# Optimization experiments

Measured on AMD Instinct MI355X. Metric: run time of the kernel, lower is better.

## Reference

```python
import jax, jax.numpy as jnp
import numpy as np
import math

B, S, D_MODEL = 2, 2048, 1024
H = 16
DK = D_MODEL // H          # 64, down-proj per-stream dim
NOPE, ROPE = 128, 64
D_HEAD = NOPE + ROPE       # 192 = d_latent // H
D_LATENT = H * D_HEAD      # 3072
ROT_DIM = 2 * ((ROPE // 2) // 2)  # rotary dim actually rotated = qk_rope_dim//2 = 32
EPS = 1e-6


def _rmsnorm(x, w):
    out = x * jax.lax.rsqrt(jnp.mean(x * x, axis=-1, keepdims=True) + EPS)
    return out * w


def _apply_rope(x):
    # x: [b, h, s, d]; rotate first ROT_DIM channels, interleaved pairing
    s = x.shape[-2]
    inv_freq = 1.0 / (10000.0 ** (jnp.arange(0, ROT_DIM, 2, dtype=jnp.float32) / ROT_DIM))
    freqs = jnp.arange(s, dtype=jnp.float32)[:, None] * inv_freq[None, :]  # [s, ROT_DIM//2]
    freqs = jnp.repeat(freqs, 2, axis=-1)  # [s, ROT_DIM], (f0,f0,f1,f1,...)
    cos, sin = jnp.cos(freqs), jnp.sin(freqs)
    xl, xr = x[..., :ROT_DIM], x[..., ROT_DIM:]
    x1, x2 = xl[..., 0::2], xl[..., 1::2]
    rot = jnp.stack([-x2, x1], axis=-1).reshape(xl.shape)
    xl = xl * cos + rot * sin
    return jnp.concatenate([xl, xr], axis=-1)


def setup_inputs() -> dict:
    key = jax.random.key(0)
    ks = jax.random.split(key, 5)
    sc = 0.02
    x = jax.random.normal(ks[0], (B, S, D_MODEL), jnp.float32)
    mask = jnp.broadcast_to(jnp.tril(jnp.ones((S, S), jnp.int32)), (B, S, S))
    w_down = jax.random.normal(ks[1], (D_MODEL, 3 * DK), jnp.float32) * sc
    rms_w = jnp.ones((3 * DK,), jnp.float32)
    w_up = jax.random.normal(ks[2], (3 * DK, 3 * D_LATENT), jnp.float32) * sc
    w_o = jax.random.normal(ks[3], (D_LATENT, D_MODEL), jnp.float32) * sc
    return {"x": x, "mask": mask, "w_down": w_down, "rms_w": rms_w, "w_up": w_up, "w_o": w_o}


def reference(x, mask, w_down, rms_w, w_up, w_o):
    h = x @ w_down                        # [b, s, 3*dk]
    h = _rmsnorm(h, rms_w)
    qkv = h @ w_up                        # [b, s, 3*d_latent]
    q, k, v = jnp.split(qkv, 3, axis=-1)  # each [b, s, d_latent]

    def to_heads(t):
        # einops '(d h)': d outer, h inner
        return t.reshape(B, S, D_HEAD, H).transpose(0, 3, 1, 2)  # [b, h, s, d]

    q, k, v = to_heads(q), to_heads(k), to_heads(v)
    q_nope, q_rope = q[..., :NOPE], q[..., NOPE:]
    k_nope, k_rope = k[..., :NOPE], k[..., NOPE:]
    q_rope = _apply_rope(q_rope)
    k_rope = _apply_rope(k_rope)

    scores = (jnp.einsum('bhid,bhjd->bhij', q_nope, k_nope)
              + jnp.einsum('bhid,bhjd->bhij', q_rope, k_rope))
    scores = scores / math.sqrt(NOPE + ROPE)
    scores = jnp.where(mask[:, None] == 0, -1e9, scores)
    attn = jax.nn.softmax(scores, axis=-1)

    out = jnp.einsum('bhij,bhjd->bhid', attn, v)        # [b, h, s, d]
    out = out.transpose(0, 2, 1, 3).reshape(B, S, D_LATENT)  # 'b h s d -> b s (h d)'
    return out @ w_o
```

## Files before the change

kernel.cpp:

```cpp
#include <hip/hip_runtime.h>
#include <stdint.h>
#include <stddef.h>


typedef __bf16 bf16x8 __attribute__((ext_vector_type(8)));
typedef float  f32x4  __attribute__((ext_vector_type(4)));

#define MFMA16x16(a,b,c) __builtin_amdgcn_mfma_f32_16x16x32_bf16((a),(b),(c),0,0,0)

__device__ __forceinline__ uint16_t f2bf(float f){
  union { float f; uint32_t u; } v; v.f = f;
  uint32_t u = v.u + 0x7fffu + ((v.u >> 16) & 1u);
  return (uint16_t)(u >> 16);
}
__device__ __forceinline__ bf16x8 load_frag(const uint16_t* p){
  uint4 u = *reinterpret_cast<const uint4*>(p);
  return __builtin_bit_cast(bf16x8, u);
}
__device__ __forceinline__ f32x4 fzero(){
  f32x4 z = {0.f, 0.f, 0.f, 0.f};
  return z;
}
__device__ __forceinline__ uint32_t pack2(float a, float b){
  return (uint32_t)f2bf(a) | ((uint32_t)f2bf(b) << 16);
}
__device__ __forceinline__ void gl2lds16(const uint16_t* g, uint16_t* l){
  __builtin_amdgcn_global_load_lds(
      (const __attribute__((address_space(1))) uint32_t*)g,
      (__attribute__((address_space(3))) uint32_t*)l,
      16, 0, 0);
}

__global__ __launch_bounds__(256) void k_transpose_cvt(const float* __restrict__ in,
                                                       uint16_t* __restrict__ out,
                                                       int R, int C){
  __shared__ float t[32][33];
  const int tc = blockIdx.x * 32;
  const int tr = blockIdx.y * 32;
  const int j = threadIdx.x & 31, i0 = threadIdx.x >> 5;
  for(int ii = 0; ii < 4; ++ii){
    int r = i0 + ii * 8;
    t[r][j] = in[(size_t)(tr + r) * C + tc + j];
  }
  __syncthreads();
  for(int ii = 0; ii < 4; ++ii){
    int c = i0 + ii * 8;
    out[(size_t)(tc + c) * R + tr + j] = f2bf(t[j][c]);
  }
}

__global__ __launch_bounds__(256) void k_down_mfma(const float* __restrict__ x,
                                                   const uint16_t* __restrict__ wdt,
                                                   const float* __restrict__ rms_w,
                                                   uint16_t* __restrict__ h_out){
  __shared__ __align__(16) uint16_t as[32 * 64];
  __shared__ float hsq[32];
  const int tid  = threadIdx.x;
  const int wave = tid >> 6, lane = tid & 63;
  const int ml = lane & 15, qd = lane >> 4;
  const int m0 = blockIdx.x * 32;
  const int n0w = wave * 48;
  if(tid < 32) hsq[tid] = 0.f;

  f32x4 acc[2][3];
#pragma unroll
  for(int mt = 0; mt < 2; ++mt)
#pragma unroll
    for(int nt = 0; nt < 3; ++nt) acc[mt][nt] = fzero();

  const int srow = tid >> 3, sc = tid & 7;
  for(int kt = 0; kt < 16; ++kt){
    const float* src = x + (size_t)(m0 + srow) * 1024 + kt * 64 + sc * 8;
    float4 a = *reinterpret_cast<const float4*>(src);
    float4 b = *reinterpret_cast<const float4*>(src + 4);
    uint4 pk;
    pk.x = pack2(a.x, a.y); pk.y = pack2(a.z, a.w);
    pk.z = pack2(b.x, b.y); pk.w = pack2(b.z, b.w);
    __syncthreads();
    *reinterpret_cast<uint4*>(as + srow * 64 + ((sc ^ (srow & 7)) * 8)) = pk;
    __syncthreads();
#pragma unroll
    for(int kk = 0; kk < 2; ++kk){
      bf16x8 af[2];
#pragma unroll
      for(int mt = 0; mt < 2; ++mt){
        int row = mt * 16 + ml;
        af[mt] = load_frag(as + row * 64 + (((kk * 4 + qd) ^ (row & 7)) * 8));
      }
#pragma unroll
      for(int nt = 0; nt < 3; ++nt){
        bf16x8 bfr = load_frag(wdt + (size_t)(n0w + nt * 16 + ml) * 1024 + kt * 64 + kk * 32 + qd * 8);
#pragma unroll
        for(int mt = 0; mt < 2; ++mt)
          acc[mt][nt] = MFMA16x16(af[mt], bfr, acc[mt][nt]);
      }
    }
  }
  __syncthreads();
#pragma unroll
  for(int mt = 0; mt < 2; ++mt)
#pragma unroll
    for(int r = 0; r < 4; ++r){
      float s = acc[mt][0][r]*acc[mt][0][r] + acc[mt][1][r]*acc[mt][1][r] + acc[mt][2][r]*acc[mt][2][r];
#pragma unroll
      for(int off = 1; off < 16; off <<= 1) s += __shfl_xor(s, off);
      if(ml == 0) atomicAdd(&hsq[mt * 16 + qd * 4 + r], s);
    }
  __syncthreads();
  float rw[3];
#pragma unroll
  for(int nt = 0; nt < 3; ++nt) rw[nt] = rms_w[n0w + nt * 16 + ml];
#pragma unroll
  for(int mt = 0; mt < 2; ++mt)
#pragma unroll
    for(int r = 0; r < 4; ++r){
      int row = mt * 16 + qd * 4 + r;
      float scl = rsqrtf(hsq[row] * (1.0f / 192.0f) + 1e-6f);
#pragma unroll
      for(int nt = 0; nt < 3; ++nt)
        h_out[(size_t)(m0 + row) * 192 + n0w + nt * 16 + ml] = f2bf(acc[mt][nt][r] * scl * rw[nt]);
    }
}

__global__ __launch_bounds__(256) void k_gemm_up(const uint16_t* __restrict__ hmat,
                                                 const uint16_t* __restrict__ wt,
                                                 uint16_t* __restrict__ q_t,
                                                 uint16_t* __restrict__ k_t,
                                                 uint16_t* __restrict__ v_t){
  __shared__ __align__(16) uint16_t rp[16 * 129 * 8];
  const int wave = threadIdx.x >> 6, lane = threadIdx.x & 63;
  const int ml = lane & 15, qd = lane >> 4;
  const int m0 = blockIdx.y * 32;
  const int bx = blockIdx.x;
  const int which = bx / 6;
  const int d0b = (bx % 6) * 32;
  const int n0w = bx * 512 + wave * 128;
  const int d0w = d0b + wave * 8;

  bf16x8 af[2][6];
#pragma unroll
  for(int mt = 0; mt < 2; ++mt)
#pragma unroll
    for(int kk = 0; kk < 6; ++kk)
      af[mt][kk] = load_frag(hmat + (size_t)(m0 + mt * 16 + ml) * 192 + kk * 32 + qd * 8);

  f32x4 acc[8][2];
#pragma unroll
  for(int nt = 0; nt < 8; ++nt){ acc[nt][0] = fzero(); acc[nt][1] = fzero(); }
#pragma unroll
  for(int nt = 0; nt < 8; ++nt){
#pragma unroll
    for(int kk = 0; kk < 6; ++kk){
      bf16x8 b = load_frag(wt + (size_t)(n0w + nt * 16 + ml) * 192 + kk * 32 + qd * 8);
      acc[nt][0] = MFMA16x16(af[0][kk], b, acc[nt][0]);
      acc[nt][1] = MFMA16x16(af[1][kk], b, acc[nt][1]);
    }
  }

  const int b   = m0 >> 11;
  const int s0  = m0 & 2047;
  const int kt2 = s0 >> 6;
  const int row0 = s0 & 63;
  uint4* rp4 = (uint4*)rp;

  if(which < 2){
    const float qs = which ? 1.0f : 0.07216878364870322f;
    const bool rope = (d0w >= 128) && (d0w < 160);
#pragma unroll
    for(int mt = 0; mt < 2; ++mt)
#pragma unroll
      for(int r = 0; r < 4; ++r){
        int t = mt * 16 + qd * 4 + r;
        int s = s0 + t;
        float v[8];
#pragma unroll
        for(int nt = 0; nt < 8; ++nt) v[nt] = acc[nt][mt][r] * qs;
        if(rope){
#pragma unroll
          for(int pi = 0; pi < 4; ++pi){
            int fi = (d0w + 2 * pi - 128) >> 1;
            float invf = __expf(-(float)fi * 0.5756462732485114f);
            float sn, cs;
            sincosf((float)s * invf, &sn, &cs);
            float e = v[2 * pi], o = v[2 * pi + 1];
            v[2 * pi]     = e * cs - o * sn;
            v[2 * pi + 1] = o * cs + e * sn;
          }
        }
        uint4 pk;
        pk.x = pack2(v[0], v[1]); pk.y = pack2(v[2], v[3]);
        pk.z = pack2(v[4], v[5]); pk.w = pack2(v[6], v[7]);
        rp4[ml * 129 + t * 4 + (wave ^ (t & 3))] = pk;
      }
  } else {
#pragma unroll
    for(int nt = 0; nt < 8; ++nt){
      int dl = wave * 8 + nt;
#pragma unroll
      for(int mt = 0; mt < 2; ++mt){
        int jc = mt * 2 + (qd >> 1);
        int slot = ml * 129 + dl * 4 + (jc ^ (dl & 3));
        uint2 pk;
        pk.x = pack2(acc[nt][mt][0], acc[nt][mt][1]);
        pk.y = pack2(acc[nt][mt][2], acc[nt][mt][3]);
        *(reinterpret_cast<uint2*>(rp + slot * 8) + (qd & 1)) = pk;
      }
    }
  }
  __syncthreads();

  if(which < 2){
    uint16_t* dst = which ? k_t : q_t;
    const int cb = d0b >> 3;
#pragma unroll
    for(int it = 0; it < 8; ++it){
      int h = wave * 4 + (it & 3), rhalf = it >> 2;
      int tloc = rhalf * 16 + (lane >> 2), p = lane & 3;
      int row = row0 + tloc;
      uint4 val = rp4[h * 129 + tloc * 4 + p];
      size_t off = ((size_t)(b * 16 + h) * 32 + kt2) * 12288
                 + (size_t)row * 192 + ((cb ^ (tloc & 4)) + p) * 8;
      *reinterpret_cast<uint4*>(dst + off) = val;
    }
  } else {
    const int cs0 = row0 >> 3;
#pragma unroll
    for(int it = 0; it < 8; ++it){
      int h = wave * 4 + (it & 3), dhalf = it >> 2;
      int dl = dhalf * 16 + (lane >> 2), p = lane & 3;
      uint4 val = rp4[h * 129 + dl * 4 + p];
      size_t off = ((size_t)(b * 16 + h) * 32 + kt2) * 12288
                 + (size_t)(d0b + dl) * 64 + ((cs0 ^ (dl & 4)) + p) * 8;
      *reinterpret_cast<uint4*>(v_t + off) = val;
    }
  }
}

__global__ __launch_bounds__(256, 3) void k_attn(const uint16_t* __restrict__ q_t,
                                                 const uint16_t* __restrict__ k_t,
                                                 const uint16_t* __restrict__ v_t,
                                                 uint16_t* __restrict__ attn_out){
  __shared__ __align__(16) uint16_t ks[64 * 192];
  __shared__ __align__(16) uint16_t vs[208 * 64];
  const int tid  = threadIdx.x;
  const int wave = tid >> 6;
  const int lane = tid & 63;
  const int ml   = lane & 15;
  const int qd   = lane >> 4;
  const int L    = blockIdx.x;
  const int idx  = L >> 3;
  const int qt   = 31 - (idx & 31);
  const int bh   = (L & 7) + ((idx >> 5) << 3);

  {
    uint32_t* vw = (uint32_t*)vs;
    vw[6144 + tid] = 0x3F803F80u;
    vw[6400 + tid] = 0x3F803F80u;
  }

  {
    const uint16_t* qtile = q_t + ((size_t)bh * 32 + qt) * (64 * 192);
#pragma unroll
    for(int it = 0; it < 6; ++it){
      int seg = it * 4 + wave;
      gl2lds16(qtile + seg * 512 + lane * 8, ks + seg * 512);
    }
  }
  __syncthreads();
  bf16x8 qf[6];
  {
    int row = wave * 16 + ml;
#pragma unroll
    for(int kk = 0; kk < 6; ++kk)
      qf[kk] = load_frag(ks + row * 192 + (((kk * 4 + qd) ^ (row & 7)) * 8));
  }

  f32x4 o[13];
#pragma unroll
  for(int i = 0; i < 13; ++i) o[i] = fzero();

  for(int kt = 0; kt <= qt; ++kt){
    __syncthreads();
    const uint16_t* ktile = k_t + ((size_t)bh * 32 + kt) * (64 * 192);
    const uint16_t* vtile = v_t + ((size_t)bh * 32 + kt) * (192 * 64);
#pragma unroll
    for(int it = 0; it < 6; ++it){
      int seg = it * 4 + wave;
      gl2lds16(ktile + seg * 512 + lane * 8, ks + seg * 512);
    }
#pragma unroll
    for(int it = 0; it < 6; ++it){
      int seg = it * 4 + wave;
      gl2lds16(vtile + seg * 512 + lane * 8, vs + seg * 512);
    }
    __syncthreads();

    float p[4][4];
    const bool diag = (kt == qt);
#pragma unroll
    for(int nt = 0; nt < 4; ++nt){
      f32x4 a = fzero();
      int row = nt * 16 + ml;
#pragma unroll
      for(int kk = 0; kk < 6; ++kk){
        bf16x8 b = load_frag(ks + row * 192 + (((kk * 4 + qd) ^ (row & 7)) * 8));
        a = MFMA16x16(qf[kk], b, a);
      }
#pragma unroll
      for(int r = 0; r < 4; ++r){
        float v = a[r];
        if(diag){
          int i = qt * 64 + wave * 16 + qd * 4 + r;
          int j = kt * 64 + nt * 16 + ml;
          if(j > i) v = -1e9f;
        }
        p[nt][r] = __expf(v);
      }
    }

    __syncthreads();
    uint16_t* psw = ks + wave * 1024;
#pragma unroll
    for(int nt = 0; nt < 4; ++nt)
#pragma unroll
      for(int r = 0; r < 4; ++r){
        int rp2 = qd * 4 + r;
        int col = nt * 16 + ml;
        int c = (col >> 3) ^ (rp2 & 7);
        psw[rp2 * 64 + c * 8 + (col & 7)] = f2bf(p[nt][r]);
      }
#pragma unroll
    for(int kk2 = 0; kk2 < 2; ++kk2){
      int cp = (kk2 * 4 + qd) ^ (ml & 7);
      bf16x8 pa = load_frag(psw + ml * 64 + cp * 8);
#pragma unroll
      for(int dt = 0; dt < 13; ++dt){
        int row = dt * 16 + ml;
        int cv = (kk2 * 4 + qd) ^ (row & 7);
        bf16x8 vb = load_frag(vs + row * 64 + cv * 8);
        o[dt] = MFMA16x16(pa, vb, o[dt]);
      }
    }
  }

  const int hh = bh & 15, b = bh >> 4;
#pragma unroll
  for(int r = 0; r < 4; ++r){
    int i = qt * 64 + wave * 16 + qd * 4 + r;
    float inv = 1.0f / o[12][r];
    size_t obase = ((size_t)b * 2048 + i) * 3072 + hh * 192;
#pragma unroll
    for(int dt = 0; dt < 12; ++dt)
      attn_out[obase + dt * 16 + ml] = f2bf(o[dt][r] * inv);
  }
}

__global__ __launch_bounds__(256) void k_gemm_o_tile(const uint16_t* __restrict__ a,
                                                     const uint16_t* __restrict__ wt,
                                                     float* __restrict__ part){
  __shared__ __align__(16) uint16_t as[128 * 64];
  __shared__ __align__(16) uint16_t bs[128 * 64];
  const int wave = threadIdx.x >> 6, lane = threadIdx.x & 63;
  const int ml = lane & 15, qd = lane >> 4;
  const int m0 = blockIdx.y * 128, n0 = blockIdx.x * 128;
  const int kz = blockIdx.z;
  const int mo = (wave >> 1) * 64, no = (wave & 1) * 64;

  const int lrow = lane >> 3;
  const int gch  = (lane & 7) ^ (lrow & 7);
  const uint16_t* abase = a  + (size_t)(m0 + lrow) * 3072 + kz * 1536 + gch * 8;
  const uint16_t* bbase = wt + (size_t)(n0 + lrow) * 3072 + kz * 1536 + gch * 8;

  f32x4 acc[4][4];
#pragma unroll
  for(int mt = 0; mt < 4; ++mt)
#pragma unroll
    for(int nt = 0; nt < 4; ++nt) acc[mt][nt] = fzero();

  for(int kt = 0; kt < 24; ++kt){
    __syncthreads();
#pragma unroll
    for(int it = 0; it < 4; ++it){
      int seg = it * 4 + wave;
      gl2lds16(abase + (size_t)seg * 24576 + kt * 64, as + seg * 512);
      gl2lds16(bbase + (size_t)seg * 24576 + kt * 64, bs + seg * 512);
    }
    __syncthreads();
#pragma unroll
    for(int ks2 = 0; ks2 < 2; ++ks2){
      bf16x8 af[4], bfr[4];
#pragma unroll
      for(int mt = 0; mt < 4; ++mt){
        int row = mo + mt * 16 + ml;
        af[mt] = load_frag(as + row * 64 + (((ks2 * 4 + qd) ^ (row & 7)) * 8));
      }
#pragma unroll
      for(int nt = 0; nt < 4; ++nt){
        int row = no + nt * 16 + ml;
        bfr[nt] = load_frag(bs + row * 64 + (((ks2 * 4 + qd) ^ (row & 7)) * 8));
      }
#pragma unroll
      for(int mt = 0; mt < 4; ++mt)
#pragma unroll
        for(int nt = 0; nt < 4; ++nt)
          acc[mt][nt] = MFMA16x16(af[mt], bfr[nt], acc[mt][nt]);
    }
  }

  float* dst = part + (size_t)kz * 4096 * 1024;
#pragma unroll
  for(int mt = 0; mt < 4; ++mt)
#pragma unroll
    for(int nt = 0; nt < 4; ++nt)
#pragma unroll
      for(int r = 0; r < 4; ++r){
        int row = m0 + mo + mt * 16 + qd * 4 + r;
        int col = n0 + no + nt * 16 + ml;
        dst[(size_t)row * 1024 + col] = acc[mt][nt][r];
      }
}

__global__ __launch_bounds__(256) void k_addout(const float* __restrict__ part,
                                                float* __restrict__ out){
  int i = blockIdx.x * 256 + threadIdx.x;
  const float4* p0 = (const float4*)part;
  const float4* p1 = p0 + (size_t)1048576;
  float4 a = p0[i], b = p1[i];
  float4 c; c.x = a.x + b.x; c.y = a.y + b.y; c.z = a.z + b.z; c.w = a.w + b.w;
  ((float4*)out)[i] = c;
}


extern "C" void kernel_launch(void* const* d_in, const int* in_sizes, int n_in,
                              void* d_out, int out_size, void* d_ws, size_t ws_size,
                              hipStream_t stream) {
  (void)in_sizes; (void)n_in; (void)out_size; (void)ws_size;
  const float* x      = (const float*)d_in[0];
  const float* w_down = (const float*)d_in[2];
  const float* rms_w  = (const float*)d_in[3];
  const float* w_up   = (const float*)d_in[4];
  const float* w_o    = (const float*)d_in[5];
  float* out = (float*)d_out;

  char* ws = (char*)d_ws;
  uint16_t* h_bf   = (uint16_t*)(ws);
  uint16_t* w_up_t = (uint16_t*)(ws + 1572864);
  uint16_t* w_o_t  = (uint16_t*)(ws + 5111808);
  uint16_t* w_dn_t = (uint16_t*)(ws + 11403264);
  uint16_t* q_tb   = (uint16_t*)(ws + 11796480);
  uint16_t* k_tb   = (uint16_t*)(ws + 36962304);
  uint16_t* v_tb   = (uint16_t*)(ws + 62128128);
  uint16_t* attnO  = (uint16_t*)(ws + 87293952);
  float*    part   = (float*)(ws + 11796480);

  k_transpose_cvt<<<dim3(288, 6), 256, 0, stream>>>(w_up, w_up_t, 192, 9216);
  k_transpose_cvt<<<dim3(32, 96), 256, 0, stream>>>(w_o,  w_o_t,  3072, 1024);
  k_transpose_cvt<<<dim3(6, 32),  256, 0, stream>>>(w_down, w_dn_t, 1024, 192);
  k_down_mfma<<<128, 256, 0, stream>>>(x, w_dn_t, rms_w, h_bf);
  k_gemm_up<<<dim3(18, 128), 256, 0, stream>>>(h_bf, w_up_t, q_tb, k_tb, v_tb);
  k_attn<<<1024, 256, 0, stream>>>(q_tb, k_tb, v_tb, attnO);
  k_gemm_o_tile<<<dim3(8, 32, 2), 256, 0, stream>>>(attnO, w_o_t, part);
  k_addout<<<4096, 256, 0, stream>>>(part, out);
}
```

Measured before the change: 354.0 us.

## Double-buffer K/V tiles in attention with 128-row query blocks and paired causal scheduling

The attention kernel now uses 512-thread blocks, each handling a 128-row query block with 8 waves. K/V tiles are double-buffered in LDS so the next tile's loads overlap compute, with explicit vmcnt waits and raised wave priority around the MFMA sections. Each block processes a pair of query blocks (15-pr and pr) to even out causal work, and the grid drops from 1024 to 256 blocks. In exchange, LDS use per block grows, occupancy drops to 2 blocks per CU, and with only 256 blocks some CUs may be left idle.

```diff
diff --git a/kernel.cpp b/kernel.cpp
--- a/kernel.cpp
+++ b/kernel.cpp
@@ -236,123 +236,176 @@
   }
 }
 
-__global__ __launch_bounds__(256, 3) void k_attn(const uint16_t* __restrict__ q_t,
+__global__ __launch_bounds__(512, 2) void k_attn(const uint16_t* __restrict__ q_t,
                                                  const uint16_t* __restrict__ k_t,
                                                  const uint16_t* __restrict__ v_t,
                                                  uint16_t* __restrict__ attn_out){
-  __shared__ __align__(16) uint16_t ks[64 * 192];
-  __shared__ __align__(16) uint16_t vs[208 * 64];
+  __shared__ __align__(16) uint16_t kb[2][64 * 192];
+  __shared__ __align__(16) uint16_t vb[2][208 * 64];
+  __shared__ __align__(16) uint16_t psw_all[8][16 * 64];
   const int tid  = threadIdx.x;
   const int wave = tid >> 6;
   const int lane = tid & 63;
   const int ml   = lane & 15;
   const int qd   = lane >> 4;
-  const int L    = blockIdx.x;
-  const int idx  = L >> 3;
-  const int qt   = 31 - (idx & 31);
-  const int bh   = (L & 7) + ((idx >> 5) << 3);
+  const int bh   = blockIdx.x & 31;
+  const int pr   = blockIdx.x >> 5;
 
   {
-    uint32_t* vw = (uint32_t*)vs;
-    vw[6144 + tid] = 0x3F803F80u;
-    vw[6400 + tid] = 0x3F803F80u;
-  }
-
-  {
-    const uint16_t* qtile = q_t + ((size_t)bh * 32 + qt) * (64 * 192);
-#pragma unroll
-    for(int it = 0; it < 6; ++it){
-      int seg = it * 4 + wave;
-      gl2lds16(qtile + seg * 512 + lane * 8, ks + seg * 512);
-    }
-  }
-  __syncthreads();
-  bf16x8 qf[6];
-  {
-    int row = wave * 16 + ml;
-#pragma unroll
-    for(int kk = 0; kk < 6; ++kk)
-      qf[kk] = load_frag(ks + row * 192 + (((kk * 4 + qd) ^ (row & 7)) * 8));
-  }
-
-  f32x4 o[13];
-#pragma unroll
-  for(int i = 0; i < 13; ++i) o[i] = fzero();
-
-  for(int kt = 0; kt <= qt; ++kt){
-    __syncthreads();
-    const uint16_t* ktile = k_t + ((size_t)bh * 32 + kt) * (64 * 192);
-    const uint16_t* vtile = v_t + ((size_t)bh * 32 + kt) * (192 * 64);
-#pragma unroll
-    for(int it = 0; it < 6; ++it){
-      int seg = it * 4 + wave;
-      gl2lds16(ktile + seg * 512 + lane * 8, ks + seg * 512);
-    }
-#pragma unroll
-    for(int it = 0; it < 6; ++it){
-      int seg = it * 4 + wave;
-      gl2lds16(vtile + seg * 512 + lane * 8, vs + seg * 512);
-    }
-    __syncthreads();
-
-    float p[4][4];
-    const bool diag = (kt == qt);
-#pragma unroll
-    for(int nt = 0; nt < 4; ++nt){
-      f32x4 a = fzero();
-      int row = nt * 16 + ml;
-#pragma unroll
-      for(int kk = 0; kk < 6; ++kk){
-        bf16x8 b = load_frag(ks + row * 192 + (((kk * 4 + qd) ^ (row & 7)) * 8));
-        a = MFMA16x16(qf[kk], b, a);
-      }
-#pragma unroll
-      for(int r = 0; r < 4; ++r){
-        float v = a[r];
-        if(diag){
-          int i = qt * 64 + wave * 16 + qd * 4 + r;
-          int j = kt * 64 + nt * 16 + ml;
-          if(j > i) v = -1e9f;
+    uint32_t* v0 = (uint32_t*)(vb[0] + 192 * 64);
+    uint32_t* v1 = (uint32_t*)(vb[1] + 192 * 64);
+    v0[tid] = 0x3F803F80u;
+    v1[tid] = 0x3F803F80u;
+  }
+
+  const uint16_t* kbase = k_t + (size_t)bh * 32 * 12288;
+  const uint16_t* vbase = v_t + (size_t)bh * 32 * 12288;
+  const uint16_t* qbase = q_t + (size_t)bh * 32 * 12288;
+  const int hh = bh & 15, bb = bh >> 4;
+
+  auto qblock = [&](int qb){
+    const int last = 2 * qb + 1;
+    {
+#pragma unroll
+      for(int it = 0; it < 3; ++it){
+        int seg = it * 8 + wave;
+        gl2lds16(kbase + seg * 512 + lane * 8, kb[0] + seg * 512);
+      }
+#pragma unroll
+      for(int it = 0; it < 3; ++it){
+        int seg = it * 8 + wave;
+        gl2lds16(vbase + seg * 512 + lane * 8, vb[0] + seg * 512);
+      }
+      const uint16_t* qt0 = qbase + (size_t)qb * 2 * 12288;
+#pragma unroll
+      for(int it = 0; it < 6; ++it){
+        int seg = it * 8 + wave;
+        uint16_t* dst = (seg < 24) ? (kb[1] + seg * 512) : (vb[1] + (seg - 24) * 512);
+        gl2lds16(qt0 + seg * 512 + lane * 8, dst);
+      }
+    }
+    __builtin_amdgcn_sched_barrier(0);
+    asm volatile("s_waitcnt vmcnt(0) lgkmcnt(0)" ::: "memory");
+    __builtin_amdgcn_sched_barrier(0);
+    __builtin_amdgcn_s_barrier();
+
+    bf16x8 qf[6];
+    {
+      int row = wave * 16 + ml;
+      const uint16_t* qsrc = (row < 64) ? (kb[1] + row * 192)
+                                        : (vb[1] + (row - 64) * 192);
+#pragma unroll
+      for(int kk = 0; kk < 6; ++kk)
+        qf[kk] = load_frag(qsrc + (((kk * 4 + qd) ^ (row & 7)) * 8));
+    }
+    asm volatile("s_waitcnt lgkmcnt(0)" ::: "memory");
+    __builtin_amdgcn_sched_barrier(0);
+    __builtin_amdgcn_s_barrier();
+
+    f32x4 o[13];
+#pragma unroll
+    for(int i = 0; i < 13; ++i) o[i] = fzero();
+
+    const int r0 = qb * 128 + wave * 16;
+    int cur = 0;
+    for(int kt = 0; kt <= last; ++kt){
+      if(kt < last){
+        const uint16_t* kn = kbase + (size_t)(kt + 1) * 12288;
+        const uint16_t* vn = vbase + (size_t)(kt + 1) * 12288;
+#pragma unroll
+        for(int it = 0; it < 3; ++it){
+          int seg = it * 8 + wave;
+          gl2lds16(kn + seg * 512 + lane * 8, kb[cur ^ 1] + seg * 512);
         }
-        p[nt][r] = __expf(v);
-      }
-    }
-
-    __syncthreads();
-    uint16_t* psw = ks + wave * 1024;
-#pragma unroll
-    for(int nt = 0; nt < 4; ++nt)
-#pragma unroll
-      for(int r = 0; r < 4; ++r){
-        int rp2 = qd * 4 + r;
-        int col = nt * 16 + ml;
-        int c = (col >> 3) ^ (rp2 & 7);
-        psw[rp2 * 64 + c * 8 + (col & 7)] = f2bf(p[nt][r]);
-      }
-#pragma unroll
-    for(int kk2 = 0; kk2 < 2; ++kk2){
-      int cp = (kk2 * 4 + qd) ^ (ml & 7);
-      bf16x8 pa = load_frag(psw + ml * 64 + cp * 8);
-#pragma unroll
-      for(int dt = 0; dt < 13; ++dt){
-        int row = dt * 16 + ml;
-        int cv = (kk2 * 4 + qd) ^ (row & 7);
-        bf16x8 vb = load_frag(vs + row * 64 + cv * 8);
-        o[dt] = MFMA16x16(pa, vb, o[dt]);
-      }
-    }
-  }
-
-  const int hh = bh & 15, b = bh >> 4;
-#pragma unroll
-  for(int r = 0; r < 4; ++r){
-    int i = qt * 64 + wave * 16 + qd * 4 + r;
-    float inv = 1.0f / o[12][r];
-    size_t obase = ((size_t)b * 2048 + i) * 3072 + hh * 192;
-#pragma unroll
-    for(int dt = 0; dt < 12; ++dt)
-      attn_out[obase + dt * 16 + ml] = f2bf(o[dt][r] * inv);
-  }
+#pragma unroll
+        for(int it = 0; it < 3; ++it){
+          int seg = it * 8 + wave;
+          gl2lds16(vn + seg * 512 + lane * 8, vb[cur ^ 1] + seg * 512);
+        }
+        __builtin_amdgcn_sched_barrier(0);
+        asm volatile("s_waitcnt vmcnt(6)" ::: "memory");
+        __builtin_amdgcn_sched_barrier(0);
+      } else {
+        asm volatile("s_waitcnt vmcnt(0)" ::: "memory");
+        __builtin_amdgcn_sched_barrier(0);
+      }
+      __builtin_amdgcn_s_barrier();
+
+      const int lo = kt * 64;
+      if(lo <= r0 + 15){
+        const bool diag = (lo + 63 > r0);
+        float p[4][4];
+        const uint16_t* kc = kb[cur];
+        __builtin_amdgcn_s_setprio(1);
+#pragma unroll
+        for(int nt = 0; nt < 4; ++nt){
+          f32x4 a = fzero();
+          int row = nt * 16 + ml;
+#pragma unroll
+          for(int kk = 0; kk < 6; ++kk){
+            bf16x8 b = load_frag(kc + row * 192 + (((kk * 4 + qd) ^ (row & 7)) * 8));
+            a = MFMA16x16(qf[kk], b, a);
+          }
+#pragma unroll
+          for(int r = 0; r < 4; ++r) p[nt][r] = a[r];
+        }
+        __builtin_amdgcn_s_setprio(0);
+#pragma unroll
+        for(int nt = 0; nt < 4; ++nt)
+#pragma unroll
+          for(int r = 0; r < 4; ++r){
+            float v = p[nt][r];
+            if(diag){
+              int i = r0 + qd * 4 + r;
+              int j = lo + nt * 16 + ml;
+              if(j > i) v = -1e9f;
+            }
+            p[nt][r] = __expf(v);
+          }
+        uint16_t* psw = psw_all[wave];
+#pragma unroll
+        for(int nt = 0; nt < 4; ++nt)
+#pragma unroll
+          for(int r = 0; r < 4; ++r){
+            int rp2 = qd * 4 + r;
+            int col = nt * 16 + ml;
+            int c = (col >> 3) ^ (rp2 & 7);
+            psw[rp2 * 64 + c * 8 + (col & 7)] = f2bf(p[nt][r]);
+          }
+        const uint16_t* vc = vb[cur];
+        __builtin_amdgcn_s_setprio(1);
+#pragma unroll
+        for(int kk2 = 0; kk2 < 2; ++kk2){
+          int cp = (kk2 * 4 + qd) ^ (ml & 7);
+          bf16x8 pa = load_frag(psw + ml * 64 + cp * 8);
+#pragma unroll
+          for(int dt = 0; dt < 13; ++dt){
+            int row = dt * 16 + ml;
+            int cv = (kk2 * 4 + qd) ^ (row & 7);
+            bf16x8 vbf = load_frag(vc + row * 64 + cv * 8);
+            o[dt] = MFMA16x16(pa, vbf, o[dt]);
+          }
+        }
+        __builtin_amdgcn_s_setprio(0);
+      }
+      __builtin_amdgcn_s_barrier();
+      cur ^= 1;
+    }
+
+#pragma unroll
+    for(int r = 0; r < 4; ++r){
+      int i = r0 + qd * 4 + r;
+      float inv = 1.0f / o[12][r];
+      size_t obase = ((size_t)bb * 2048 + i) * 3072 + hh * 192;
+#pragma unroll
+      for(int dt = 0; dt < 12; ++dt)
+        attn_out[obase + dt * 16 + ml] = f2bf(o[dt][r] * inv);
+    }
+  };
+
+  qblock(15 - pr);
+  qblock(pr);
+  asm volatile("s_waitcnt vmcnt(0)" ::: "memory");
 }
 
 __global__ __launch_bounds__(256) void k_gemm_o_tile(const uint16_t* __restrict__ a,
@@ -458,7 +511,7 @@
   k_transpose_cvt<<<dim3(6, 32),  256, 0, stream>>>(w_down, w_dn_t, 1024, 192);
   k_down_mfma<<<128, 256, 0, stream>>>(x, w_dn_t, rms_w, h_bf);
   k_gemm_up<<<dim3(18, 128), 256, 0, stream>>>(h_bf, w_up_t, q_tb, k_tb, v_tb);
-  k_attn<<<1024, 256, 0, stream>>>(q_tb, k_tb, v_tb, attnO);
+  k_attn<<<256, 512, 0, stream>>>(q_tb, k_tb, v_tb, attnO);
   k_gemm_o_tile<<<dim3(8, 32, 2), 256, 0, stream>>>(attnO, w_o_t, part);
   k_addout<<<4096, 256, 0, stream>>>(part, out);
 }
```

New measurement: 337.5 us. -4.7%, faster.
